# Kernel optimization log

Measured on AMD Instinct MI355X. Metric: run time of the kernel, lower is better.

The kernel has to match this reference:

```python
import jax, jax.numpy as jnp
import numpy as np

EPS = 1e-5

def conv2d(x, w, b, stride, pad):
    y = jax.lax.conv_general_dilated(x, w, (stride, stride), [(pad, pad), (pad, pad)],
                                     dimension_numbers=('NCHW', 'OIHW', 'NCHW'))
    return y + b[None, :, None, None]

def _sample(xb, py, px):
    # xb: [C,H,W]; py,px: [K,Ho,Wo] fractional sample coords (zero padding outside)
    H, W = xb.shape[1], xb.shape[2]
    y0 = jnp.floor(py); x0 = jnp.floor(px)
    ay = py - y0; ax = px - x0
    y0i = y0.astype(jnp.int32); x0i = x0.astype(jnp.int32)
    out = jnp.zeros((xb.shape[0],) + py.shape, xb.dtype)
    for dy, wy in ((0, 1.0 - ay), (1, ay)):
        for dx, wx in ((0, 1.0 - ax), (1, ax)):
            yi = y0i + dy; xi = x0i + dx
            valid = (yi >= 0) & (yi < H) & (xi >= 0) & (xi < W)
            v = xb[:, jnp.clip(yi, 0, H - 1), jnp.clip(xi, 0, W - 1)]  # [C,K,Ho,Wo]
            out = out + v * (wy * wx * valid)[None]
    return out

def deform_conv2d(x, w, offset, mask, stride, pad):
    # torchvision.ops.deform_conv2d semantics (modulated, 1 offset group)
    B, C, H, W = x.shape
    Co, Ci, kh, kw = w.shape
    K = kh * kw
    Ho = (H + 2 * pad - kh) // stride + 1
    Wo = (W + 2 * pad - kw) // stride + 1
    ky, kx = jnp.meshgrid(jnp.arange(kh), jnp.arange(kw), indexing='ij')
    ky = ky.reshape(K).astype(x.dtype); kx = kx.reshape(K).astype(x.dtype)
    off = offset.reshape(B, K, 2, Ho, Wo)  # channel 2k = dy, 2k+1 = dx
    base_y = (jnp.arange(Ho) * stride - pad).astype(x.dtype)
    base_x = (jnp.arange(Wo) * stride - pad).astype(x.dtype)
    py = base_y[None, None, :, None] + ky[None, :, None, None] + off[:, :, 0]
    px = base_x[None, None, None, :] + kx[None, :, None, None] + off[:, :, 1]
    cols = jax.vmap(_sample)(x, py, px)        # [B,C,K,Ho,Wo]
    cols = cols * mask[:, None]                # modulated
    return jnp.einsum('bckhw,ock->bohw', cols, w.reshape(Co, Ci, K))

def deform_layer(x, off_w, off_b, mod_w, mod_b, w, stride, pad):
    offset = conv2d(x, off_w, off_b, stride, pad)
    mask = 2.0 * jax.nn.sigmoid(conv2d(x, mod_w, mod_b, stride, pad))
    return deform_conv2d(x, w, offset, mask, stride, pad)

def bn(x, g, b, m, v):
    return (x - m[None, :, None, None]) * (g / jnp.sqrt(v + EPS))[None, :, None, None] + b[None, :, None, None]

def prelu(x, alpha):
    return jnp.where(x > 0, x, alpha[None, :, None, None] * x)

def setup_inputs() -> dict:
    key = jax.random.key(0)
    ks = jax.random.split(key, 24)
    B, C, D, H, W, k = 4, 128, 128, 128, 128, 3
    K = k * k
    n = lambda i, shp, s: jax.random.normal(ks[i], shp, dtype=jnp.float32) * s
    inp = {
        'x': n(0, (B, C, H, W), 1.0),
        'bn1_g': 1.0 + n(1, (C,), 0.05), 'bn1_b': n(2, (C,), 0.05),
        'bn1_m': n(3, (C,), 0.1), 'bn1_v': jax.random.uniform(ks[4], (C,), jnp.float32, 0.5, 1.5),
        'off1_w': n(5, (2 * K, C, k, k), 0.01), 'off1_b': n(6, (2 * K,), 0.01),
        'mod1_w': n(7, (K, C, k, k), 0.01), 'mod1_b': n(8, (K,), 0.01),
        'w1': n(9, (D, C, k, k), 1.0 / np.sqrt(C * K)),
        'alpha': jnp.full((D,), 0.25, jnp.float32),
        'off2_w': n(10, (2 * K, D, k, k), 0.01), 'off2_b': n(11, (2 * K,), 0.01),
        'mod2_w': n(12, (K, D, k, k), 0.01), 'mod2_b': n(13, (K,), 0.01),
        'w2': n(14, (D, D, k, k), 1.0 / np.sqrt(D * K)),
        'bn2_g': 1.0 + n(15, (D,), 0.05), 'bn2_b': n(16, (D,), 0.05),
        'bn2_m': n(17, (D,), 0.1), 'bn2_v': jax.random.uniform(ks[18], (D,), jnp.float32, 0.5, 1.5),
    }
    return inp

def reference(x, bn1_g, bn1_b, bn1_m, bn1_v, off1_w, off1_b, mod1_w, mod1_b, w1, alpha,
              off2_w, off2_b, mod2_w, mod2_b, w2, bn2_g, bn2_b, bn2_m, bn2_v):
    # in_channel == depth, stride == 1 -> shortcut is MaxPool2d(1,1) == identity
    shortcut = x
    r = bn(x, bn1_g, bn1_b, bn1_m, bn1_v)
    r = deform_layer(r, off1_w, off1_b, mod1_w, mod1_b, w1, 1, 1)
    r = prelu(r, alpha)
    r = deform_layer(r, off2_w, off2_b, mod2_w, mod2_b, w2, 1, 1)
    r = bn(r, bn2_g, bn2_b, bn2_m, bn2_v)
    return r + shortcut
```

## Files before the change

kernel.cpp:

```cpp
#include <hip/hip_runtime.h>
#include <hip/hip_bf16.h>
#include <hip/hip_fp16.h>
#include <math.h>

#define DEV_INLINE __device__ __forceinline__

typedef __attribute__((ext_vector_type(8))) short short8;
typedef __attribute__((ext_vector_type(8))) unsigned short ushort8v;
typedef __attribute__((ext_vector_type(4))) float f32x4;

constexpr int H = 128, W = 128, C = 128, B = 4;
constexpr int KK = 9;
constexpr int KT2 = 1184;
constexpr int GP = 80;
constexpr int GHALF = 64 * GP;

DEV_INLINE unsigned short f2bf(float f) {
  union { float f; unsigned u; } v; v.f = f;
  unsigned r = v.u + 0x7FFFu + ((v.u >> 16) & 1u);
  return (unsigned short)(r >> 16);
}
DEV_INLINE float ubits(unsigned u) {
  union { unsigned u; float f; } v; v.u = u; return v.f;
}
DEV_INLINE unsigned pack2bf(float a, float b) {
  float2 t; t.x = a; t.y = b;
  __hip_bfloat162 h = __float22bfloat162_rn(t);
  union { __hip_bfloat162 h; unsigned u; } c; c.h = h;
  return c.u;
}
DEV_INLINE unsigned f2h2(float a, float b) {
  __half2 h = __floats2half2_rn(a, b);
  union { __half2 h; unsigned u; } c; c.h = h;
  return c.u;
}
DEV_INLINE float2 h2f2(unsigned u) {
  union { unsigned u; __half2 h; } c; c.u = u;
  return __half22float2(c.h);
}
DEV_INLINE unsigned blend4(unsigned TL, unsigned TR, unsigned BL, unsigned BR,
                           float w00, float w01, float w10, float w11) {
  const float lo = w00 * ubits(TL << 16) + w01 * ubits(TR << 16)
                 + w10 * ubits(BL << 16) + w11 * ubits(BR << 16);
  const float hi = w00 * ubits(TL & 0xFFFF0000u) + w01 * ubits(TR & 0xFFFF0000u)
                 + w10 * ubits(BL & 0xFFFF0000u) + w11 * ubits(BR & 0xFFFF0000u);
  return pack2bf(lo, hi);
}
DEV_INLINE void lgkm_barrier() {
  asm volatile("s_waitcnt lgkmcnt(0)" ::: "memory");
  __builtin_amdgcn_s_barrier();
  __builtin_amdgcn_sched_barrier(0);
}

template<int LAYER>
__global__ __launch_bounds__(256, 4)
void fusedL(const unsigned short* __restrict__ src,
            const unsigned short* __restrict__ wOM,
            const unsigned short* __restrict__ wS,
            const float* __restrict__ bias,
            const float* __restrict__ pA, const float* __restrict__ pB,
            const float* __restrict__ pM, const float* __restrict__ pV,
            const float* __restrict__ resid,
            unsigned short* __restrict__ outh,
            float* __restrict__ outf)
{
  constexpr bool BN   = (LAYER == 1);
  constexpr int  NCH3 = BN ? 37 : 36;
  __shared__ __attribute__((aligned(16))) char smem[17152];
  char* gBuf = smem;
  float* sOff = (float*)smem;
  unsigned* sTabU = (unsigned*)(smem + 10240);

  const int tid  = threadIdx.x;
  const int lane = tid & 63;
  const int m16  = lane & 15;
  const int q    = lane >> 4;
  const int wv   = tid >> 6;

  const int raw  = blockIdx.x;
  const int xcd  = raw & 7;
  const int slot = raw >> 3;
  const int b    = xcd >> 1;
  const int hy   = ((xcd & 1) << 6) | (slot >> 1);
  const int hx0  = (slot & 1) << 6;
  const unsigned short* __restrict__ srcB = src + ((size_t)b << 14) * C;

  const int pos  = (wv << 4) + m16;
  const int ppos = tid >> 2;
  const int ps   = tid & 3;

  f32x4 acc2[2];
  acc2[0] = (f32x4){0.f, 0.f, 0.f, 0.f};
  acc2[1] = (f32x4){0.f, 0.f, 0.f, 0.f};

  {
    const int iy = hy - 1, ix = hx0 + ppos - 1;
    uint4 v; v.x = 0; v.y = 0; v.z = 0; v.w = 0;
    if (((unsigned)iy < (unsigned)H) && ((unsigned)ix < (unsigned)W))
      v = *(const uint4*)(srcB + (size_t)(iy * W + ix) * C + (ps << 3));
    *(uint4*)(gBuf + ppos * GP + (ps << 4)) = v;
  }
  uint4 pendV; pendV.x = 0; pendV.y = 0; pendV.z = 0; pendV.w = 0;
  {
    const int iy = hy - 1, ix = hx0 + ppos - 1;
    if (((unsigned)iy < (unsigned)H) && ((unsigned)ix < (unsigned)W))
      pendV = *(const uint4*)(srcB + (size_t)(iy * W + ix) * C + 32 + (ps << 3));
  }
  short8 pa0 = *(const short8*)(wOM + (size_t)lane * 8);
  short8 pa1 = *(const short8*)(wOM + (size_t)lane * 8 + 512);
  lgkm_barrier();

  #pragma unroll 2
  for (int ch = 0; ch < 36; ++ch) {
    const int p = ch & 1;
    const short8 a0 = pa0, a1 = pa1;
    if (ch + 1 < 36) {
      const unsigned short* ap = wOM + ((size_t)((ch + 1) * 128 + lane)) * 8;
      pa0 = *(const short8*)(ap);
      pa1 = *(const short8*)(ap + 512);
    }
    uint4 newV; newV.x = 0; newV.y = 0; newV.z = 0; newV.w = 0;
    if (ch + 2 < 36) {
      const int t2 = (ch + 2) >> 2, c2 = (ch + 2) & 3;
      const int ky = t2 / 3, kx = t2 - 3 * (t2 / 3);
      const int iy = hy + ky - 1;
      const int ix = hx0 + ppos + kx - 1;
      if (((unsigned)iy < (unsigned)H) && ((unsigned)ix < (unsigned)W))
        newV = *(const uint4*)(srcB + (size_t)(iy * W + ix) * C + (c2 << 5) + (ps << 3));
    }
    if (ch + 1 < 36)
      *(uint4*)(gBuf + (p ^ 1) * GHALF + ppos * GP + (ps << 4)) = pendV;
    const short8 bfrg = *(const short8*)(gBuf + p * GHALF + pos * GP + (q << 4));
    acc2[0] = __builtin_amdgcn_mfma_f32_16x16x32_bf16(a0, bfrg, acc2[0], 0, 0, 0);
    acc2[1] = __builtin_amdgcn_mfma_f32_16x16x32_bf16(a1, bfrg, acc2[1], 0, 0, 0);
    pendV = newV;
    if (ch + 1 < 36) lgkm_barrier();
  }
  if constexpr (BN) {
    union { unsigned u[4]; short8 s; } bfr;
    float sv[8];
    #pragma unroll
    for (int j = 0; j < 8; ++j) {
      const int kj = (q << 3) + j;
      float s = 0.f;
      if (kj < KK) {
        const int ky = kj / 3, kx = kj - 3 * (kj / 3);
        const int iy = hy + ky - 1, ix = hx0 + pos + kx - 1;
        s = (((unsigned)iy < (unsigned)H) && ((unsigned)ix < (unsigned)W)) ? 1.f : 0.f;
      }
      sv[j] = s;
    }
    #pragma unroll
    for (int t = 0; t < 4; ++t) bfr.u[t] = pack2bf(sv[2 * t], sv[2 * t + 1]);
    const unsigned short* ap = wOM + ((size_t)36 * 128 + lane) * 8;
    acc2[0] = __builtin_amdgcn_mfma_f32_16x16x32_bf16(*(const short8*)(ap), bfr.s, acc2[0], 0, 0, 0);
    acc2[1] = __builtin_amdgcn_mfma_f32_16x16x32_bf16(*(const short8*)(ap + 512), bfr.s, acc2[1], 0, 0, 0);
  }
  __syncthreads();
  #pragma unroll
  for (int ot = 0; ot < 2; ++ot) {
    #pragma unroll
    for (int rg = 0; rg < 4; ++rg) {
      const int o = ot * 16 + (q << 2) + rg;
      if (o < 27) {
        float v = acc2[ot][rg] + bias[o];
        if (o >= 18) v = 2.f / (1.f + expf(-v));
        sOff[pos * 29 + o] = v;
      }
    }
  }
  __syncthreads();

  {
    const float* myOff = sOff + pos * 29;
    #pragma unroll
    for (int tap = 0; tap < 9; ++tap) {
      const int ky = tap / 3, kx = tap - 3 * (tap / 3);
      const float oy = myOff[2 * tap];
      const float ox = myOff[2 * tap + 1];
      const float mv = myOff[18 + tap];
      const float py = (float)(hy - 1 + ky) + oy;
      const float px = (float)(hx0 + pos - 1 + kx) + ox;
      const float fy = floorf(py), fx = floorf(px);
      const float ay = py - fy, ax = px - fx;
      const int y0 = (int)fy, x0 = (int)fx;
      const int y1 = y0 + 1, x1 = x0 + 1;
      const float wyt = (1.f - ay) * (((unsigned)y0 < (unsigned)H) ? 1.f : 0.f);
      const float wyb = ay * (((unsigned)y1 < (unsigned)H) ? 1.f : 0.f);
      const int y0c = min(max(y0, 0), H - 1), y1c = min(max(y1, 0), H - 1);
      const int bx  = min(max(x0, 0), W - 2);
      float wA = 0.f, wB = 0.f;
      if (x0 == bx)          { wA = 1.f - ax; wB = ax; }
      else if (x1 == bx)     { wA = ax; }
      else if (x0 == bx + 1) { wB = 1.f - ax; }
      if (q == 0) {
        const int tb = (tap * 64 + pos) * 3;
        sTabU[tb + 0] = (unsigned)(y0c * W + bx) | ((unsigned)(y1c * W + bx) << 16);
        sTabU[tb + 1] = f2h2(mv * wyt * wA, mv * wyt * wB);
        sTabU[tb + 2] = f2h2(mv * wyb * wA, mv * wyb * wB);
      }
    }
  }
  __syncthreads();

  f32x4 acc[2][4];
  #pragma unroll
  for (int i = 0; i < 2; ++i)
    #pragma unroll
    for (int j = 0; j < 4; ++j) acc[i][j] = (f32x4){0.f, 0.f, 0.f, 0.f};

  unsigned tabId, tabW0, tabW1;
  {
    const int tb = ppos * 3;
    tabId = sTabU[tb]; tabW0 = sTabU[tb + 1]; tabW1 = sTabU[tb + 2];
  }
  {
    const unsigned short* pT  = srcB + (size_t)(tabId & 0xFFFFu) * C + (ps << 3);
    const unsigned short* pBm = srcB + (size_t)(tabId >> 16) * C + (ps << 3);
    const uint4 TL = *(const uint4*)(pT),  TR = *(const uint4*)(pT + C);
    const uint4 BL = *(const uint4*)(pBm), BR = *(const uint4*)(pBm + C);
    const float2 wa = h2f2(tabW0), wb = h2f2(tabW1);
    uint4 o;
    o.x = blend4(TL.x, TR.x, BL.x, BR.x, wa.x, wa.y, wb.x, wb.y);
    o.y = blend4(TL.y, TR.y, BL.y, BR.y, wa.x, wa.y, wb.x, wb.y);
    o.z = blend4(TL.z, TR.z, BL.z, BR.z, wa.x, wa.y, wb.x, wb.y);
    o.w = blend4(TL.w, TR.w, BL.w, BR.w, wa.x, wa.y, wb.x, wb.y);
    *(uint4*)(gBuf + ppos * GP + (ps << 4)) = o;
  }
  uint4 pTL, pTR, pBL, pBR;
  {
    const int cbn = 32 + (ps << 3);
    const unsigned short* pT  = srcB + (size_t)(tabId & 0xFFFFu) * C + cbn;
    const unsigned short* pBm = srcB + (size_t)(tabId >> 16) * C + cbn;
    pTL = *(const uint4*)(pT);  pTR = *(const uint4*)(pT + C);
    pBL = *(const uint4*)(pBm); pBR = *(const uint4*)(pBm + C);
  }
  short8 pa0_, pa1_;
  {
    const unsigned short* ap = wS + ((size_t)((2 * wv) * 64 + lane)) * 8;
    pa0_ = *(const short8*)(ap);
    pa1_ = *(const short8*)(ap + 512);
  }
  lgkm_barrier();

  #pragma unroll 2
  for (int ch = 0; ch < 36; ++ch) {
    const int p = ch & 1;
    const short8 af0 = pa0_, af1 = pa1_;
    if (ch + 1 < NCH3) {
      const unsigned short* ap = wS + ((size_t)((ch + 1) * 4096)) +
                                 ((size_t)((2 * wv) * 64 + lane)) * 8;
      pa0_ = *(const short8*)(ap);
      pa1_ = *(const short8*)(ap + 512);
    }
    unsigned ntId = tabId, ntW0 = tabW0, ntW1 = tabW1;
    if ((((ch + 2) & 3) == 0) && (ch + 2 < 36)) {
      const int tb = (((ch + 2) >> 2) * 64 + ppos) * 3;
      ntId = sTabU[tb]; ntW0 = sTabU[tb + 1]; ntW1 = sTabU[tb + 2];
    }
    uint4 nTL = pTL, nTR = pTR, nBL = pBL, nBR = pBR;
    if (ch + 2 < 36) {
      const int cbn = (((ch + 2) & 3) << 5) + (ps << 3);
      const unsigned short* pT  = srcB + (size_t)(ntId & 0xFFFFu) * C + cbn;
      const unsigned short* pBm = srcB + (size_t)(ntId >> 16) * C + cbn;
      nTL = *(const uint4*)(pT);  nTR = *(const uint4*)(pT + C);
      nBL = *(const uint4*)(pBm); nBR = *(const uint4*)(pBm + C);
    }
    if (ch + 1 < 36) {
      const float2 wa = h2f2(tabW0), wb = h2f2(tabW1);
      uint4 o;
      o.x = blend4(pTL.x, pTR.x, pBL.x, pBR.x, wa.x, wa.y, wb.x, wb.y);
      o.y = blend4(pTL.y, pTR.y, pBL.y, pBR.y, wa.x, wa.y, wb.x, wb.y);
      o.z = blend4(pTL.z, pTR.z, pBL.z, pBR.z, wa.x, wa.y, wb.x, wb.y);
      o.w = blend4(pTL.w, pTR.w, pBL.w, pBR.w, wa.x, wa.y, wb.x, wb.y);
      *(uint4*)(gBuf + (p ^ 1) * GHALF + ppos * GP + (ps << 4)) = o;
    }
    const char* gb = gBuf + p * GHALF;
    short8 bf[4];
    #pragma unroll
    for (int pg = 0; pg < 4; ++pg)
      bf[pg] = *(const short8*)(gb + (pg * 16 + m16) * GP + (q << 4));
    #pragma unroll
    for (int pg = 0; pg < 4; ++pg) {
      acc[0][pg] = __builtin_amdgcn_mfma_f32_16x16x32_bf16(af0, bf[pg], acc[0][pg], 0, 0, 0);
      acc[1][pg] = __builtin_amdgcn_mfma_f32_16x16x32_bf16(af1, bf[pg], acc[1][pg], 0, 0, 0);
    }
    pTL = nTL; pTR = nTR; pBL = nBL; pBR = nBR;
    tabId = ntId; tabW0 = ntW0; tabW1 = ntW1;
    if (ch + 1 < 36) lgkm_barrier();
  }

  if constexpr (BN) {
    const short8 af0 = pa0_, af1 = pa1_;
    #pragma unroll
    for (int pg = 0; pg < 4; ++pg) {
      float sv[8];
      #pragma unroll
      for (int j = 0; j < 8; ++j) {
        const int k = (q << 3) + j;
        float s = 0.f;
        if (k < KK) {
          const int tb = (k * 64 + pg * 16 + m16) * 3;
          const float2 a = h2f2(sTabU[tb + 1]);
          const float2 c = h2f2(sTabU[tb + 2]);
          s = a.x + a.y + c.x + c.y;
        }
        sv[j] = s;
      }
      union { unsigned u[4]; short8 s; } bfr;
      #pragma unroll
      for (int t = 0; t < 4; ++t) bfr.u[t] = pack2bf(sv[2 * t], sv[2 * t + 1]);
      acc[0][pg] = __builtin_amdgcn_mfma_f32_16x16x32_bf16(af0, bfr.s, acc[0][pg], 0, 0, 0);
      acc[1][pg] = __builtin_amdgcn_mfma_f32_16x16x32_bf16(af1, bfr.s, acc[1][pg], 0, 0, 0);
    }
  }

  #pragma unroll
  for (int oi = 0; oi < 2; ++oi) {
    const int ot = wv * 2 + oi;
    if constexpr (LAYER == 1) {
      const float a0 = pA[ot * 16 + (q << 2) + 0];
      const float a1 = pA[ot * 16 + (q << 2) + 1];
      const float a2 = pA[ot * 16 + (q << 2) + 2];
      const float a3 = pA[ot * 16 + (q << 2) + 3];
      #pragma unroll
      for (int pg = 0; pg < 4; ++pg) {
        const float v0 = acc[oi][pg][0], v1 = acc[oi][pg][1];
        const float v2 = acc[oi][pg][2], v3 = acc[oi][pg][3];
        uint2 st;
        st.x = pack2bf(v0 > 0.f ? v0 : a0 * v0, v1 > 0.f ? v1 : a1 * v1);
        st.y = pack2bf(v2 > 0.f ? v2 : a2 * v2, v3 > 0.f ? v3 : a3 * v3);
        const int n = (b << 14) + hy * W + hx0 + pg * 16 + m16;
        *(uint2*)(outh + (size_t)n * C + ot * 16 + (q << 2)) = st;
      }
    } else {
      #pragma unroll
      for (int rg = 0; rg < 4; ++rg) {
        const int o = ot * 16 + (q << 2) + rg;
        const float s  = pA[o] * rsqrtf(pV[o] + 1e-5f);
        const float sh = pB[o] - pM[o] * s;
        #pragma unroll
        for (int pg = 0; pg < 4; ++pg) {
          const size_t oi2 = (((size_t)(b * C + o)) << 14) + hy * W + hx0 + pg * 16 + m16;
          outf[oi2] = acc[oi][pg][rg] * s + sh + resid[oi2];
        }
      }
    }
  }
}

__global__ __launch_bounds__(256, 4)
void xcvt3(const float* __restrict__ x, unsigned short* __restrict__ xb)
{
  __shared__ unsigned tile[64 * 69];
  const int b   = blockIdx.y;
  const int p0  = blockIdx.x * 64;
  const int tid = threadIdx.x;
  const int pl  = tid & 63;
  const int cg  = tid >> 6;
  const float* __restrict__ xp = x + (((size_t)(b * C) + cg * 32) << 14) + p0 + pl;
  #pragma unroll
  for (int j = 0; j < 16; ++j) {
    const float a = xp[(size_t)(2 * j) << 14];
    const float c = xp[(size_t)(2 * j + 1) << 14];
    tile[pl * 69 + cg * 16 + j] = pack2bf(a, c);
  }
  __syncthreads();
  const int pl2 = tid >> 2;
  const int cq  = tid & 3;
  unsigned* dst = (unsigned*)(xb + (((size_t)(b << 14)) + p0 + pl2) * C + cq * 32);
  #pragma unroll
  for (int k = 0; k < 16; k += 4) {
    uint4 v;
    v.x = tile[pl2 * 69 + cq * 16 + k];
    v.y = tile[pl2 * 69 + cq * 16 + k + 1];
    v.z = tile[pl2 * 69 + cq * 16 + k + 2];
    v.w = tile[pl2 * 69 + cq * 16 + k + 3];
    *(uint4*)(dst + k) = v;
  }
}

__global__ void prep5(const float* __restrict__ w1, const float* __restrict__ w2,
                      const float* __restrict__ ow1, const float* __restrict__ mw1,
                      const float* __restrict__ ob1, const float* __restrict__ mb1,
                      const float* __restrict__ ow2, const float* __restrict__ mw2,
                      const float* __restrict__ ob2, const float* __restrict__ mb2,
                      const float* __restrict__ g, const float* __restrict__ bb,
                      const float* __restrict__ m, const float* __restrict__ v,
                      unsigned short* __restrict__ wb1, unsigned short* __restrict__ wb2,
                      unsigned short* __restrict__ wom1, unsigned short* __restrict__ wom2,
                      float* __restrict__ bias1, float* __restrict__ bias2)
{
  const int i = blockIdx.x * 256 + threadIdx.x;
  if (i < 128 * KT2) {
    const int j = i & 7, lane = (i >> 3) & 63, ot = (i >> 9) & 7, ch = i >> 12;
    const int o = ot * 16 + (lane & 15);
    const int qj = ((lane >> 4) << 3) + j;
    unsigned short v1 = 0, v2 = 0;
    if (ch < 36) {
      const int tap = ch >> 2;
      const int c   = ((ch & 3) << 5) + qj;
      const float s = g[c] * rsqrtf(v[c] + 1e-5f);
      v1 = f2bf(w1[(size_t)(o * 128 + c) * 9 + tap] * s);
      v2 = f2bf(w2[(size_t)(o * 128 + c) * 9 + tap]);
    } else if (qj < KK) {
      float acc = 0.f;
      for (int c = 0; c < 128; ++c) {
        const float s  = g[c] * rsqrtf(v[c] + 1e-5f);
        const float sh = bb[c] - m[c] * s;
        acc += w1[(size_t)(o * 128 + c) * 9 + qj] * sh;
      }
      v1 = f2bf(acc);
    }
    wb1[i] = v1; wb2[i] = v2;
  }
  if (i < 32 * KT2) {
    const int j = i & 7, lane = (i >> 3) & 63, ot = (i >> 9) & 1, ch = i >> 10;
    const int o = ot * 16 + (lane & 15);
    const int qj = ((lane >> 4) << 3) + j;
    unsigned short v1 = 0, v2 = 0;
    if (ch < 36) {
      const int tap = ch >> 2;
      const int c   = ((ch & 3) << 5) + qj;
      const float s = g[c] * rsqrtf(v[c] + 1e-5f);
      if (o < 18) {
        v1 = f2bf(ow1[(size_t)(o * 128 + c) * 9 + tap] * s);
        v2 = f2bf(ow2[(size_t)(o * 128 + c) * 9 + tap]);
      } else if (o < 27) {
        v1 = f2bf(mw1[(size_t)((o - 18) * 128 + c) * 9 + tap] * s);
        v2 = f2bf(mw2[(size_t)((o - 18) * 128 + c) * 9 + tap]);
      }
    } else if (qj < KK && o < 27) {
      const float* wsrc = (o < 18) ? ow1 + (size_t)o * 1152
                                   : mw1 + (size_t)(o - 18) * 1152;
      float acc = 0.f;
      for (int c = 0; c < 128; ++c) {
        const float s  = g[c] * rsqrtf(v[c] + 1e-5f);
        const float sh = bb[c] - m[c] * s;
        acc += wsrc[(size_t)c * 9 + qj] * sh;
      }
      v1 = f2bf(acc);
    }
    wom1[i] = v1; wom2[i] = v2;
  }
  if (i < 32) {
    float b1 = 0.f, b2 = 0.f;
    if (i < 18)      { b1 = ob1[i];      b2 = ob2[i]; }
    else if (i < 27) { b1 = mb1[i - 18]; b2 = mb2[i - 18]; }
    bias1[i] = b1; bias2[i] = b2;
  }
}

extern "C" void kernel_launch(void* const* d_in, const int* in_sizes, int n_in,
                              void* d_out, int out_size, void* d_ws, size_t ws_size,
                              hipStream_t stream)
{
  const float* x     = (const float*)d_in[0];
  const float* bn1g  = (const float*)d_in[1];
  const float* bn1b  = (const float*)d_in[2];
  const float* bn1m  = (const float*)d_in[3];
  const float* bn1v  = (const float*)d_in[4];
  const float* ow1   = (const float*)d_in[5];
  const float* ob1   = (const float*)d_in[6];
  const float* mw1   = (const float*)d_in[7];
  const float* mb1   = (const float*)d_in[8];
  const float* w1    = (const float*)d_in[9];
  const float* alpha = (const float*)d_in[10];
  const float* ow2   = (const float*)d_in[11];
  const float* ob2   = (const float*)d_in[12];
  const float* mw2   = (const float*)d_in[13];
  const float* mb2   = (const float*)d_in[14];
  const float* w2    = (const float*)d_in[15];
  const float* bn2g  = (const float*)d_in[16];
  const float* bn2b  = (const float*)d_in[17];
  const float* bn2m  = (const float*)d_in[18];
  const float* bn2v  = (const float*)d_in[19];
  float* out = (float*)d_out;

  char* wsp = (char*)d_ws;
  unsigned short* xbf  = (unsigned short*)(wsp);
  unsigned short* r2bf = (unsigned short*)(wsp + 16777216);
  unsigned short* wb1  = (unsigned short*)(wsp + 40632320);
  unsigned short* wb2  = (unsigned short*)(wsp + 40935424);
  unsigned short* wom1 = (unsigned short*)(wsp + 41238528);
  unsigned short* wom2 = (unsigned short*)(wsp + 41314304);
  float* bias1 = (float*)(wsp + 41390080);
  float* bias2 = (float*)(wsp + 41390208);

  xcvt3<<<dim3(256, 4), 256, 0, stream>>>(x, xbf);
  prep5<<<(128 * KT2 + 255) / 256, 256, 0, stream>>>(
      w1, w2, ow1, mw1, ob1, mb1, ow2, mw2, ob2, mb2,
      bn1g, bn1b, bn1m, bn1v, wb1, wb2, wom1, wom2, bias1, bias2);

  fusedL<1><<<1024, 256, 0, stream>>>(xbf, wom1, wb1, bias1, alpha,
      nullptr, nullptr, nullptr, nullptr, r2bf, nullptr);
  fusedL<2><<<1024, 256, 0, stream>>>(r2bf, wom2, wb2, bias2, bn2g,
      bn2b, bn2m, bn2v, x, nullptr, out);
}
```

Measured before the change: 257.7 us.

## Shrink fused deform kernel to single-wave blocks and drop barriers

Each block now covers 16 pixels with one 64-lane wave instead of 64 pixels with four waves, launched as 4096 blocks. Because the whole block is a single wave, the LDS barriers between the offset conv, table build and sampling GEMM stages are removed. Each wave now computes all 8 output tiles, loading weight fragments directly each chunk rather than software-prefetching them. The trade is more redundant offset-conv weight loads per pixel, more accumulator registers, and less weight reuse per block, in exchange for no barrier stalls and finer scheduling.

```diff
diff --git a/kernel.cpp b/kernel.cpp
--- a/kernel.cpp
+++ b/kernel.cpp
@@ -6,14 +6,13 @@
 #define DEV_INLINE __device__ __forceinline__
 
 typedef __attribute__((ext_vector_type(8))) short short8;
-typedef __attribute__((ext_vector_type(8))) unsigned short ushort8v;
 typedef __attribute__((ext_vector_type(4))) float f32x4;
 
 constexpr int H = 128, W = 128, C = 128, B = 4;
 constexpr int KK = 9;
 constexpr int KT2 = 1184;
 constexpr int GP = 80;
-constexpr int GHALF = 64 * GP;
+constexpr int G1 = 16 * GP;
 
 DEV_INLINE unsigned short f2bf(float f) {
   union { float f; unsigned u; } v; v.f = f;
@@ -46,14 +45,9 @@
                  + w10 * ubits(BL & 0xFFFF0000u) + w11 * ubits(BR & 0xFFFF0000u);
   return pack2bf(lo, hi);
 }
-DEV_INLINE void lgkm_barrier() {
-  asm volatile("s_waitcnt lgkmcnt(0)" ::: "memory");
-  __builtin_amdgcn_s_barrier();
-  __builtin_amdgcn_sched_barrier(0);
-}
 
 template<int LAYER>
-__global__ __launch_bounds__(256, 4)
+__global__ __launch_bounds__(64, 4)
 void fusedL(const unsigned short* __restrict__ src,
             const unsigned short* __restrict__ wOM,
             const unsigned short* __restrict__ wS,
@@ -64,51 +58,45 @@
             unsigned short* __restrict__ outh,
             float* __restrict__ outf)
 {
-  constexpr bool BN   = (LAYER == 1);
-  constexpr int  NCH3 = BN ? 37 : 36;
-  __shared__ __attribute__((aligned(16))) char smem[17152];
+  constexpr bool BN = (LAYER == 1);
+  __shared__ __attribute__((aligned(16))) char smem[6144];
   char* gBuf = smem;
-  float* sOff = (float*)smem;
-  unsigned* sTabU = (unsigned*)(smem + 10240);
-
-  const int tid  = threadIdx.x;
-  const int lane = tid & 63;
+  unsigned* sTabU = (unsigned*)(smem + 2560);
+  float* sOff = (float*)(smem + 4288);
+
+  const int lane = threadIdx.x;
   const int m16  = lane & 15;
   const int q    = lane >> 4;
-  const int wv   = tid >> 6;
+  const int pp   = lane >> 2;
+  const int ps   = lane & 3;
 
   const int raw  = blockIdx.x;
   const int xcd  = raw & 7;
   const int slot = raw >> 3;
   const int b    = xcd >> 1;
-  const int hy   = ((xcd & 1) << 6) | (slot >> 1);
-  const int hx0  = (slot & 1) << 6;
+  const int hy   = ((xcd & 1) << 6) | (slot >> 3);
+  const int hx0  = (slot & 7) << 4;
   const unsigned short* __restrict__ srcB = src + ((size_t)b << 14) * C;
-
-  const int pos  = (wv << 4) + m16;
-  const int ppos = tid >> 2;
-  const int ps   = tid & 3;
 
   f32x4 acc2[2];
   acc2[0] = (f32x4){0.f, 0.f, 0.f, 0.f};
   acc2[1] = (f32x4){0.f, 0.f, 0.f, 0.f};
 
   {
-    const int iy = hy - 1, ix = hx0 + ppos - 1;
+    const int iy = hy - 1, ix = hx0 + pp - 1;
     uint4 v; v.x = 0; v.y = 0; v.z = 0; v.w = 0;
     if (((unsigned)iy < (unsigned)H) && ((unsigned)ix < (unsigned)W))
       v = *(const uint4*)(srcB + (size_t)(iy * W + ix) * C + (ps << 3));
-    *(uint4*)(gBuf + ppos * GP + (ps << 4)) = v;
+    *(uint4*)(gBuf + pp * GP + (ps << 4)) = v;
   }
   uint4 pendV; pendV.x = 0; pendV.y = 0; pendV.z = 0; pendV.w = 0;
   {
-    const int iy = hy - 1, ix = hx0 + ppos - 1;
+    const int iy = hy - 1, ix = hx0 + pp - 1;
     if (((unsigned)iy < (unsigned)H) && ((unsigned)ix < (unsigned)W))
       pendV = *(const uint4*)(srcB + (size_t)(iy * W + ix) * C + 32 + (ps << 3));
   }
   short8 pa0 = *(const short8*)(wOM + (size_t)lane * 8);
   short8 pa1 = *(const short8*)(wOM + (size_t)lane * 8 + 512);
-  lgkm_barrier();
 
   #pragma unroll 2
   for (int ch = 0; ch < 36; ++ch) {
@@ -124,17 +112,16 @@
       const int t2 = (ch + 2) >> 2, c2 = (ch + 2) & 3;
       const int ky = t2 / 3, kx = t2 - 3 * (t2 / 3);
       const int iy = hy + ky - 1;
-      const int ix = hx0 + ppos + kx - 1;
+      const int ix = hx0 + pp + kx - 1;
       if (((unsigned)iy < (unsigned)H) && ((unsigned)ix < (unsigned)W))
         newV = *(const uint4*)(srcB + (size_t)(iy * W + ix) * C + (c2 << 5) + (ps << 3));
     }
     if (ch + 1 < 36)
-      *(uint4*)(gBuf + (p ^ 1) * GHALF + ppos * GP + (ps << 4)) = pendV;
-    const short8 bfrg = *(const short8*)(gBuf + p * GHALF + pos * GP + (q << 4));
-    acc2[0] = __builtin_amdgcn_mfma_f32_16x16x32_bf16(a0, bfrg, acc2[0], 0, 0, 0);
-    acc2[1] = __builtin_amdgcn_mfma_f32_16x16x32_bf16(a1, bfrg, acc2[1], 0, 0, 0);
+      *(uint4*)(gBuf + (p ^ 1) * G1 + pp * GP + (ps << 4)) = pendV;
+    const short8 bf = *(const short8*)(gBuf + p * G1 + m16 * GP + (q << 4));
+    acc2[0] = __builtin_amdgcn_mfma_f32_16x16x32_bf16(a0, bf, acc2[0], 0, 0, 0);
+    acc2[1] = __builtin_amdgcn_mfma_f32_16x16x32_bf16(a1, bf, acc2[1], 0, 0, 0);
     pendV = newV;
-    if (ch + 1 < 36) lgkm_barrier();
   }
   if constexpr (BN) {
     union { unsigned u[4]; short8 s; } bfr;
@@ -145,7 +132,7 @@
       float s = 0.f;
       if (kj < KK) {
         const int ky = kj / 3, kx = kj - 3 * (kj / 3);
-        const int iy = hy + ky - 1, ix = hx0 + pos + kx - 1;
+        const int iy = hy + ky - 1, ix = hx0 + m16 + kx - 1;
         s = (((unsigned)iy < (unsigned)H) && ((unsigned)ix < (unsigned)W)) ? 1.f : 0.f;
       }
       sv[j] = s;
@@ -156,7 +143,6 @@
     acc2[0] = __builtin_amdgcn_mfma_f32_16x16x32_bf16(*(const short8*)(ap), bfr.s, acc2[0], 0, 0, 0);
     acc2[1] = __builtin_amdgcn_mfma_f32_16x16x32_bf16(*(const short8*)(ap + 512), bfr.s, acc2[1], 0, 0, 0);
   }
-  __syncthreads();
   #pragma unroll
   for (int ot = 0; ot < 2; ++ot) {
     #pragma unroll
@@ -165,14 +151,13 @@
       if (o < 27) {
         float v = acc2[ot][rg] + bias[o];
         if (o >= 18) v = 2.f / (1.f + expf(-v));
-        sOff[pos * 29 + o] = v;
-      }
-    }
-  }
-  __syncthreads();
-
-  {
-    const float* myOff = sOff + pos * 29;
+        sOff[m16 * 29 + o] = v;
+      }
+    }
+  }
+
+  {
+    const float* myOff = sOff + m16 * 29;
     #pragma unroll
     for (int tap = 0; tap < 9; ++tap) {
       const int ky = tap / 3, kx = tap - 3 * (tap / 3);
@@ -180,7 +165,7 @@
       const float ox = myOff[2 * tap + 1];
       const float mv = myOff[18 + tap];
       const float py = (float)(hy - 1 + ky) + oy;
-      const float px = (float)(hx0 + pos - 1 + kx) + ox;
+      const float px = (float)(hx0 + m16 - 1 + kx) + ox;
       const float fy = floorf(py), fx = floorf(px);
       const float ay = py - fy, ax = px - fx;
       const int y0 = (int)fy, x0 = (int)fx;
@@ -194,156 +179,139 @@
       else if (x1 == bx)     { wA = ax; }
       else if (x0 == bx + 1) { wB = 1.f - ax; }
       if (q == 0) {
-        const int tb = (tap * 64 + pos) * 3;
+        const int tb = (tap * 16 + m16) * 3;
         sTabU[tb + 0] = (unsigned)(y0c * W + bx) | ((unsigned)(y1c * W + bx) << 16);
         sTabU[tb + 1] = f2h2(mv * wyt * wA, mv * wyt * wB);
         sTabU[tb + 2] = f2h2(mv * wyb * wA, mv * wyb * wB);
       }
     }
   }
-  __syncthreads();
-
-  f32x4 acc[2][4];
+
+  f32x4 acc[8];
   #pragma unroll
-  for (int i = 0; i < 2; ++i)
-    #pragma unroll
-    for (int j = 0; j < 4; ++j) acc[i][j] = (f32x4){0.f, 0.f, 0.f, 0.f};
-
-  unsigned tabId, tabW0, tabW1;
-  {
-    const int tb = ppos * 3;
-    tabId = sTabU[tb]; tabW0 = sTabU[tb + 1]; tabW1 = sTabU[tb + 2];
-  }
-  {
-    const unsigned short* pT  = srcB + (size_t)(tabId & 0xFFFFu) * C + (ps << 3);
-    const unsigned short* pBm = srcB + (size_t)(tabId >> 16) * C + (ps << 3);
+  for (int i = 0; i < 8; ++i) acc[i] = (f32x4){0.f, 0.f, 0.f, 0.f};
+
+  unsigned wB0, wB1;
+  unsigned idI, iw0, iw1;
+  {
+    const int tb = pp * 3;
+    idI = sTabU[tb]; iw0 = sTabU[tb + 1]; iw1 = sTabU[tb + 2];
+    wB0 = iw0; wB1 = iw1;
+  }
+  {
+    const int cbn = (ps << 3);
+    const unsigned short* pT  = srcB + (size_t)(idI & 0xFFFFu) * C + cbn;
+    const unsigned short* pBm = srcB + (size_t)(idI >> 16) * C + cbn;
     const uint4 TL = *(const uint4*)(pT),  TR = *(const uint4*)(pT + C);
     const uint4 BL = *(const uint4*)(pBm), BR = *(const uint4*)(pBm + C);
-    const float2 wa = h2f2(tabW0), wb = h2f2(tabW1);
+    const float2 wa = h2f2(iw0), wb = h2f2(iw1);
     uint4 o;
     o.x = blend4(TL.x, TR.x, BL.x, BR.x, wa.x, wa.y, wb.x, wb.y);
     o.y = blend4(TL.y, TR.y, BL.y, BR.y, wa.x, wa.y, wb.x, wb.y);
     o.z = blend4(TL.z, TR.z, BL.z, BR.z, wa.x, wa.y, wb.x, wb.y);
     o.w = blend4(TL.w, TR.w, BL.w, BR.w, wa.x, wa.y, wb.x, wb.y);
-    *(uint4*)(gBuf + ppos * GP + (ps << 4)) = o;
+    *(uint4*)(gBuf + pp * GP + (ps << 4)) = o;
   }
   uint4 pTL, pTR, pBL, pBR;
   {
     const int cbn = 32 + (ps << 3);
-    const unsigned short* pT  = srcB + (size_t)(tabId & 0xFFFFu) * C + cbn;
-    const unsigned short* pBm = srcB + (size_t)(tabId >> 16) * C + cbn;
+    const unsigned short* pT  = srcB + (size_t)(idI & 0xFFFFu) * C + cbn;
+    const unsigned short* pBm = srcB + (size_t)(idI >> 16) * C + cbn;
     pTL = *(const uint4*)(pT);  pTR = *(const uint4*)(pT + C);
     pBL = *(const uint4*)(pBm); pBR = *(const uint4*)(pBm + C);
   }
-  short8 pa0_, pa1_;
-  {
-    const unsigned short* ap = wS + ((size_t)((2 * wv) * 64 + lane)) * 8;
-    pa0_ = *(const short8*)(ap);
-    pa1_ = *(const short8*)(ap + 512);
-  }
-  lgkm_barrier();
 
   #pragma unroll 2
   for (int ch = 0; ch < 36; ++ch) {
     const int p = ch & 1;
-    const short8 af0 = pa0_, af1 = pa1_;
-    if (ch + 1 < NCH3) {
-      const unsigned short* ap = wS + ((size_t)((ch + 1) * 4096)) +
-                                 ((size_t)((2 * wv) * 64 + lane)) * 8;
-      pa0_ = *(const short8*)(ap);
-      pa1_ = *(const short8*)(ap + 512);
-    }
-    unsigned ntId = tabId, ntW0 = tabW0, ntW1 = tabW1;
     if ((((ch + 2) & 3) == 0) && (ch + 2 < 36)) {
-      const int tb = (((ch + 2) >> 2) * 64 + ppos) * 3;
-      ntId = sTabU[tb]; ntW0 = sTabU[tb + 1]; ntW1 = sTabU[tb + 2];
-    }
-    uint4 nTL = pTL, nTR = pTR, nBL = pBL, nBR = pBR;
-    if (ch + 2 < 36) {
-      const int cbn = (((ch + 2) & 3) << 5) + (ps << 3);
-      const unsigned short* pT  = srcB + (size_t)(ntId & 0xFFFFu) * C + cbn;
-      const unsigned short* pBm = srcB + (size_t)(ntId >> 16) * C + cbn;
-      nTL = *(const uint4*)(pT);  nTR = *(const uint4*)(pT + C);
-      nBL = *(const uint4*)(pBm); nBR = *(const uint4*)(pBm + C);
-    }
+      const int tb = (((ch + 2) >> 2) * 16 + pp) * 3;
+      idI = sTabU[tb]; iw0 = sTabU[tb + 1]; iw1 = sTabU[tb + 2];
+    }
+    const unsigned short* apb = wS + (size_t)ch * 4096 + (size_t)lane * 8;
+    const short8 af0 = *(const short8*)(apb);
+    const short8 af1 = *(const short8*)(apb + 512);
+    const short8 af2 = *(const short8*)(apb + 1024);
+    const short8 af3 = *(const short8*)(apb + 1536);
     if (ch + 1 < 36) {
-      const float2 wa = h2f2(tabW0), wb = h2f2(tabW1);
+      const float2 wa = h2f2(wB0), wb = h2f2(wB1);
       uint4 o;
       o.x = blend4(pTL.x, pTR.x, pBL.x, pBR.x, wa.x, wa.y, wb.x, wb.y);
       o.y = blend4(pTL.y, pTR.y, pBL.y, pBR.y, wa.x, wa.y, wb.x, wb.y);
       o.z = blend4(pTL.z, pTR.z, pBL.z, pBR.z, wa.x, wa.y, wb.x, wb.y);
       o.w = blend4(pTL.w, pTR.w, pBL.w, pBR.w, wa.x, wa.y, wb.x, wb.y);
-      *(uint4*)(gBuf + (p ^ 1) * GHALF + ppos * GP + (ps << 4)) = o;
-    }
-    const char* gb = gBuf + p * GHALF;
-    short8 bf[4];
-    #pragma unroll
-    for (int pg = 0; pg < 4; ++pg)
-      bf[pg] = *(const short8*)(gb + (pg * 16 + m16) * GP + (q << 4));
-    #pragma unroll
-    for (int pg = 0; pg < 4; ++pg) {
-      acc[0][pg] = __builtin_amdgcn_mfma_f32_16x16x32_bf16(af0, bf[pg], acc[0][pg], 0, 0, 0);
-      acc[1][pg] = __builtin_amdgcn_mfma_f32_16x16x32_bf16(af1, bf[pg], acc[1][pg], 0, 0, 0);
-    }
-    pTL = nTL; pTR = nTR; pBL = nBL; pBR = nBR;
-    tabId = ntId; tabW0 = ntW0; tabW1 = ntW1;
-    if (ch + 1 < 36) lgkm_barrier();
+      *(uint4*)(gBuf + (p ^ 1) * G1 + pp * GP + (ps << 4)) = o;
+    }
+    if (ch + 2 < 36) {
+      const int cbn = (((ch + 2) & 3) << 5) + (ps << 3);
+      const unsigned short* pT  = srcB + (size_t)(idI & 0xFFFFu) * C + cbn;
+      const unsigned short* pBm = srcB + (size_t)(idI >> 16) * C + cbn;
+      pTL = *(const uint4*)(pT);  pTR = *(const uint4*)(pT + C);
+      pBL = *(const uint4*)(pBm); pBR = *(const uint4*)(pBm + C);
+    }
+    const short8 bf = *(const short8*)(gBuf + p * G1 + m16 * GP + (q << 4));
+    acc[0] = __builtin_amdgcn_mfma_f32_16x16x32_bf16(af0, bf, acc[0], 0, 0, 0);
+    acc[1] = __builtin_amdgcn_mfma_f32_16x16x32_bf16(af1, bf, acc[1], 0, 0, 0);
+    acc[2] = __builtin_amdgcn_mfma_f32_16x16x32_bf16(af2, bf, acc[2], 0, 0, 0);
+    acc[3] = __builtin_amdgcn_mfma_f32_16x16x32_bf16(af3, bf, acc[3], 0, 0, 0);
+    const short8 af4 = *(const short8*)(apb + 2048);
+    const short8 af5 = *(const short8*)(apb + 2560);
+    const short8 af6 = *(const short8*)(apb + 3072);
+    const short8 af7 = *(const short8*)(apb + 3584);
+    acc[4] = __builtin_amdgcn_mfma_f32_16x16x32_bf16(af4, bf, acc[4], 0, 0, 0);
+    acc[5] = __builtin_amdgcn_mfma_f32_16x16x32_bf16(af5, bf, acc[5], 0, 0, 0);
+    acc[6] = __builtin_amdgcn_mfma_f32_16x16x32_bf16(af6, bf, acc[6], 0, 0, 0);
+    acc[7] = __builtin_amdgcn_mfma_f32_16x16x32_bf16(af7, bf, acc[7], 0, 0, 0);
+    if (((ch + 2) & 3) == 0) { wB0 = iw0; wB1 = iw1; }
   }
 
   if constexpr (BN) {
-    const short8 af0 = pa0_, af1 = pa1_;
-    #pragma unroll
-    for (int pg = 0; pg < 4; ++pg) {
-      float sv[8];
-      #pragma unroll
-      for (int j = 0; j < 8; ++j) {
-        const int k = (q << 3) + j;
-        float s = 0.f;
-        if (k < KK) {
-          const int tb = (k * 64 + pg * 16 + m16) * 3;
-          const float2 a = h2f2(sTabU[tb + 1]);
-          const float2 c = h2f2(sTabU[tb + 2]);
-          s = a.x + a.y + c.x + c.y;
-        }
-        sv[j] = s;
-      }
-      union { unsigned u[4]; short8 s; } bfr;
-      #pragma unroll
-      for (int t = 0; t < 4; ++t) bfr.u[t] = pack2bf(sv[2 * t], sv[2 * t + 1]);
-      acc[0][pg] = __builtin_amdgcn_mfma_f32_16x16x32_bf16(af0, bfr.s, acc[0][pg], 0, 0, 0);
-      acc[1][pg] = __builtin_amdgcn_mfma_f32_16x16x32_bf16(af1, bfr.s, acc[1][pg], 0, 0, 0);
+    union { unsigned u[4]; short8 s; } bfr;
+    float sv[8];
+    #pragma unroll
+    for (int j = 0; j < 8; ++j) {
+      const int k = (q << 3) + j;
+      float s = 0.f;
+      if (k < KK) {
+        const int tb = (k * 16 + m16) * 3;
+        const float2 a = h2f2(sTabU[tb + 1]);
+        const float2 c = h2f2(sTabU[tb + 2]);
+        s = a.x + a.y + c.x + c.y;
+      }
+      sv[j] = s;
+    }
+    #pragma unroll
+    for (int t = 0; t < 4; ++t) bfr.u[t] = pack2bf(sv[2 * t], sv[2 * t + 1]);
+    const unsigned short* apb = wS + (size_t)36 * 4096 + (size_t)lane * 8;
+    #pragma unroll
+    for (int ot = 0; ot < 8; ++ot) {
+      const short8 af = *(const short8*)(apb + ot * 512);
+      acc[ot] = __builtin_amdgcn_mfma_f32_16x16x32_bf16(af, bfr.s, acc[ot], 0, 0, 0);
     }
   }
 
   #pragma unroll
-  for (int oi = 0; oi < 2; ++oi) {
-    const int ot = wv * 2 + oi;
+  for (int ot = 0; ot < 8; ++ot) {
     if constexpr (LAYER == 1) {
       const float a0 = pA[ot * 16 + (q << 2) + 0];
       const float a1 = pA[ot * 16 + (q << 2) + 1];
       const float a2 = pA[ot * 16 + (q << 2) + 2];
       const float a3 = pA[ot * 16 + (q << 2) + 3];
-      #pragma unroll
-      for (int pg = 0; pg < 4; ++pg) {
-        const float v0 = acc[oi][pg][0], v1 = acc[oi][pg][1];
-        const float v2 = acc[oi][pg][2], v3 = acc[oi][pg][3];
-        uint2 st;
-        st.x = pack2bf(v0 > 0.f ? v0 : a0 * v0, v1 > 0.f ? v1 : a1 * v1);
-        st.y = pack2bf(v2 > 0.f ? v2 : a2 * v2, v3 > 0.f ? v3 : a3 * v3);
-        const int n = (b << 14) + hy * W + hx0 + pg * 16 + m16;
-        *(uint2*)(outh + (size_t)n * C + ot * 16 + (q << 2)) = st;
-      }
+      const float v0 = acc[ot][0], v1 = acc[ot][1];
+      const float v2 = acc[ot][2], v3 = acc[ot][3];
+      uint2 st;
+      st.x = pack2bf(v0 > 0.f ? v0 : a0 * v0, v1 > 0.f ? v1 : a1 * v1);
+      st.y = pack2bf(v2 > 0.f ? v2 : a2 * v2, v3 > 0.f ? v3 : a3 * v3);
+      const int n = (b << 14) + hy * W + hx0 + m16;
+      *(uint2*)(outh + (size_t)n * C + ot * 16 + (q << 2)) = st;
     } else {
       #pragma unroll
       for (int rg = 0; rg < 4; ++rg) {
         const int o = ot * 16 + (q << 2) + rg;
         const float s  = pA[o] * rsqrtf(pV[o] + 1e-5f);
         const float sh = pB[o] - pM[o] * s;
-        #pragma unroll
-        for (int pg = 0; pg < 4; ++pg) {
-          const size_t oi2 = (((size_t)(b * C + o)) << 14) + hy * W + hx0 + pg * 16 + m16;
-          outf[oi2] = acc[oi][pg][rg] * s + sh + resid[oi2];
-        }
+        const size_t oi = (((size_t)(b * C + o)) << 14) + hy * W + hx0 + m16;
+        outf[oi] = acc[ot][rg] * s + sh + resid[oi];
       }
     }
   }
@@ -492,8 +460,8 @@
       w1, w2, ow1, mw1, ob1, mb1, ow2, mw2, ob2, mb2,
       bn1g, bn1b, bn1m, bn1v, wb1, wb2, wom1, wom2, bias1, bias2);
 
-  fusedL<1><<<1024, 256, 0, stream>>>(xbf, wom1, wb1, bias1, alpha,
+  fusedL<1><<<4096, 64, 0, stream>>>(xbf, wom1, wb1, bias1, alpha,
       nullptr, nullptr, nullptr, nullptr, r2bf, nullptr);
-  fusedL<2><<<1024, 256, 0, stream>>>(r2bf, wom2, wb2, bias2, bn2g,
+  fusedL<2><<<4096, 64, 0, stream>>>(r2bf, wom2, wb2, bias2, bn2g,
       bn2b, bn2m, bn2v, x, nullptr, out);
 }
```

New measurement: 290.7 us. 12.8% more time.
